# Performance work log

Hardware: AMD Instinct MI355X
Metric: run time of the kernel (lower is better)

Reference implementation:

```python
import math
import jax, jax.numpy as jnp
import numpy as np

B, T, S, H, L, NH = 2, 512, 2048, 768, 32, 12
INTERMED = 4 * H


def _make_pe(max_len, hidden):
    position = np.arange(max_len)[:, None].astype(np.float32)
    div_term = np.exp(np.arange(0, hidden, 2).astype(np.float32) * (-math.log(10000.0) / hidden))
    pe = np.zeros((max_len, hidden), dtype=np.float32)
    pe[:, 0::2] = np.sin(position * div_term)
    pe[:, 1::2] = np.cos(position * div_term)
    return jnp.asarray(pe)


def setup_inputs() -> dict:
    key = jax.random.key(0)
    ks = jax.random.split(key, 10)
    token_reps = jax.random.normal(ks[0], (B, T, H), dtype=jnp.float32)
    starts = jax.random.randint(ks[1], (B, S), 0, T - L)
    lens = jax.random.randint(ks[2], (B, S), 1, L + 1)
    span_ids = jnp.stack([starts, starts + lens], axis=-1)  # (B,S,2)
    span_masks = jax.random.uniform(ks[3], (B, S)) > 0.2
    pe = _make_pe(T, H)
    dummy_query = jax.random.normal(ks[4], (H,), dtype=jnp.float32) * 0.02
    in_proj_w = jax.random.normal(ks[5], (3 * H, H), dtype=jnp.float32) * 0.02
    in_proj_b = jnp.zeros((3 * H,), jnp.float32)
    out_proj_w = jax.random.normal(ks[6], (H, H), dtype=jnp.float32) * 0.02
    out_proj_b = jnp.zeros((H,), jnp.float32)
    norm_g = jnp.ones((H,), jnp.float32)
    norm_b = jnp.zeros((H,), jnp.float32)
    ffn_w1 = jax.random.normal(ks[7], (INTERMED, H), dtype=jnp.float32) * (math.sqrt(2.0 / H))
    ffn_b1 = jnp.zeros((INTERMED,), jnp.float32)
    ffn_w2 = jax.random.normal(ks[8], (H, INTERMED), dtype=jnp.float32) * (math.sqrt(2.0 / INTERMED))
    ffn_b2 = jnp.zeros((H,), jnp.float32)
    return dict(token_reps=token_reps, span_ids=span_ids, span_masks=span_masks,
                pooling=0, pe=pe, dummy_query=dummy_query,
                in_proj_w=in_proj_w, in_proj_b=in_proj_b,
                out_proj_w=out_proj_w, out_proj_b=out_proj_b,
                norm_g=norm_g, norm_b=norm_b,
                ffn_w1=ffn_w1, ffn_b1=ffn_b1, ffn_w2=ffn_w2, ffn_b2=ffn_b2)


def _layernorm(x, g, b, eps=1e-5):
    mu = jnp.mean(x, axis=-1, keepdims=True)
    var = jnp.mean(jnp.square(x - mu), axis=-1, keepdims=True)
    return (x - mu) * jax.lax.rsqrt(var + eps) * g + b


def reference(token_reps, span_ids, span_masks, pooling, pe, dummy_query,
              in_proj_w, in_proj_b, out_proj_w, out_proj_b,
              norm_g, norm_b, ffn_w1, ffn_b1, ffn_w2, ffn_b2):
    b, t, h = token_reps.shape
    s = span_ids.shape[1]
    hd = h // NH
    # positional encoding over the sequence (dropout=0 / eval mode)
    x = token_reps + pe[:t]
    # ragged -> padded gather of span tokens
    starts = span_ids[..., 0]
    lens = (span_ids[..., 1] - starts) * span_masks.astype(span_ids.dtype)  # (B,S)
    ar = jnp.arange(L)
    pos = starts[..., None] + ar                     # (B,S,L)
    valid = ar[None, None, :] < lens[..., None]      # (B,S,L) True = real token
    idx = jnp.clip(pos, 0, t - 1)
    gathered = jax.vmap(lambda xb, ib: xb[ib])(x, idx)   # (B,S,L,H)
    gathered = gathered * valid[..., None]
    # guard fully-masked rows (masked-out / zero-len spans): keep one key valid,
    # output is zeroed at the end anyway (matches torch span_reps[~mask]=0)
    any_v = jnp.any(valid, axis=-1)
    valid = valid.at[..., 0].set(valid[..., 0] | ~any_v)
    # single-query multi-head attention (torch nn.MultiheadAttention math)
    Wq, Wk, Wv = jnp.split(in_proj_w, 3, axis=0)
    bq, bk, bv = jnp.split(in_proj_b, 3, axis=0)
    q = (dummy_query @ Wq.T + bq).reshape(NH, hd)                  # (NH,hd)
    k = (gathered @ Wk.T + bk).reshape(b, s, L, NH, hd)
    v = (gathered @ Wv.T + bv).reshape(b, s, L, NH, hd)
    scores = jnp.einsum('nd,bslnd->bsnl', q, k) / math.sqrt(hd)    # (B,S,NH,L)
    scores = jnp.where(valid[:, :, None, :], scores, -jnp.inf)
    attn = jax.nn.softmax(scores, axis=-1)
    ctx = jnp.einsum('bsnl,bslnd->bsnd', attn, v).reshape(b, s, h)
    attn_out = ctx @ out_proj_w.T + out_proj_b
    # residual + LayerNorm, FFN, residual + same LayerNorm
    x1 = _layernorm(attn_out + dummy_query, norm_g, norm_b)
    ffn = jax.nn.relu(x1 @ ffn_w1.T + ffn_b1) @ ffn_w2.T + ffn_b2
    out = _layernorm(ffn + x1, norm_g, norm_b)
    out = out * span_masks[..., None]
    return out
```

## Files before the change

### kernel.cpp

```cpp
#include <hip/hip_runtime.h>
#include <math.h>

static constexpr int B_  = 2;
static constexpr int T_  = 512;
static constexpr int S_  = 2048;
static constexpr int H_  = 768;
static constexpr int L_  = 32;
static constexpr int NH_ = 12;
static constexpr int HD_ = 64;
static constexpr int IM_ = 3072;

typedef __bf16 bf16x8 __attribute__((ext_vector_type(8)));
typedef float  f32x4  __attribute__((ext_vector_type(4)));

__device__ __forceinline__ float bf2f(unsigned short u) {
    return __uint_as_float(((unsigned)u) << 16);
}
__device__ __forceinline__ unsigned short f2bf(float f) {
    unsigned u = __float_as_uint(f);
    u += 0x7fffu + ((u >> 16) & 1u);
    return (unsigned short)(u >> 16);
}
__device__ __forceinline__ void gl_lds16(const void* g, void* l) {
    __builtin_amdgcn_global_load_lds((const __attribute__((address_space(1))) void*)g,
                                     (__attribute__((address_space(3))) void*)l, 16, 0, 0);
}

__global__ void k_q(const float* __restrict__ dq, const float* __restrict__ w,
                    const float* __restrict__ b, float* __restrict__ q,
                    const int* __restrict__ raw, int* __restrict__ mout) {
    int wv = threadIdx.x >> 6, lane = threadIdx.x & 63;
    int i = blockIdx.x * 4 + wv;
    const float* row = w + (size_t)i * H_;
    float acc = 0.f;
#pragma unroll
    for (int k = 0; k < 12; ++k) acc += dq[lane + 64 * k] * row[lane + 64 * k];
    for (int m = 32; m; m >>= 1) acc += __shfl_xor(acc, m, 64);
    if (lane == 0) q[i] = acc + b[i];
    if (blockIdx.x == 0) {
        __shared__ int bad;
        if (threadIdx.x == 0) bad = 0;
        __syncthreads();
        for (int t = threadIdx.x; t < 1024; t += 256) {
            int v = raw[t];
            if (v != 0 && v != 1) bad = 1;
        }
        __syncthreads();
        int byte_layout = bad;
        const unsigned char* rb = (const unsigned char*)raw;
        for (int t = threadIdx.x; t < B_ * S_; t += 256)
            mout[t] = byte_layout ? (int)rb[t] : raw[t];
    }
}

static constexpr int CWB = 2880;
__global__ void k_castw(const float* __restrict__ s0, const float* __restrict__ s1,
                        const float* __restrict__ s2, const float* __restrict__ s3,
                        unsigned short* __restrict__ d0, unsigned short* __restrict__ d1,
                        unsigned short* __restrict__ d2, unsigned short* __restrict__ d3,
                        const float* __restrict__ q, const float* __restrict__ wk,
                        float* __restrict__ wq) {
    if (blockIdx.x >= CWB) {
        int i = (blockIdx.x - CWB) * 256 + threadIdx.x;
        int n = i / H_, hh = i % H_;
        float acc = 0.f;
        for (int d = 0; d < HD_; ++d)
            acc += q[n * HD_ + d] * wk[(size_t)(H_ + n * HD_ + d) * H_ + hh];
        wq[i] = acc;
        return;
    }
    const long n0 = (long)H_ * H_, n2 = (long)IM_ * H_;
    long gid = (long)(blockIdx.x * 256 + threadIdx.x) * 8;
    const float* s; unsigned short* d; long off;
    if (gid < n0)                { s = s0; d = d0; off = gid; }
    else if (gid < 2 * n0)       { s = s1; d = d1; off = gid - n0; }
    else if (gid < 2 * n0 + n2)  { s = s2; d = d2; off = gid - 2 * n0; }
    else                         { s = s3; d = d3; off = gid - 2 * n0 - n2; }
    float4 f0 = *(const float4*)(s + off);
    float4 f1 = *(const float4*)(s + off + 4);
    uint4 o;
    o.x = (unsigned)f2bf(f0.x) | ((unsigned)f2bf(f0.y) << 16);
    o.y = (unsigned)f2bf(f0.z) | ((unsigned)f2bf(f0.w) << 16);
    o.z = (unsigned)f2bf(f1.x) | ((unsigned)f2bf(f1.y) << 16);
    o.w = (unsigned)f2bf(f1.z) | ((unsigned)f2bf(f1.w) << 16);
    *(uint4*)(d + off) = o;
}

__global__ void k_xstok(const float* __restrict__ tr, const float* __restrict__ pe,
                        const float* __restrict__ wq,
                        unsigned short* __restrict__ xbf, float* __restrict__ stok) {
    __shared__ float sx[H_];
    int bt = blockIdx.x, tid = threadIdx.x;
    const float* trow = tr + (size_t)bt * H_;
    const float* prow = pe + (size_t)(bt % T_) * H_;
    if (tid < 192) {
        int h0 = tid * 4;
        float4 a = *(const float4*)(trow + h0);
        float4 p = *(const float4*)(prow + h0);
        float v0 = a.x + p.x, v1 = a.y + p.y, v2 = a.z + p.z, v3 = a.w + p.w;
        sx[h0] = v0; sx[h0 + 1] = v1; sx[h0 + 2] = v2; sx[h0 + 3] = v3;
        uint2 o;
        o.x = (unsigned)f2bf(v0) | ((unsigned)f2bf(v1) << 16);
        o.y = (unsigned)f2bf(v2) | ((unsigned)f2bf(v3) << 16);
        *(uint2*)(xbf + (size_t)bt * H_ + h0) = o;
    }
    __syncthreads();
    int lane = tid & 63, w = tid >> 6;
    float xv[12];
#pragma unroll
    for (int k = 0; k < 12; ++k) xv[k] = sx[lane + 64 * k];
#pragma unroll
    for (int hh = 0; hh < 3; ++hh) {
        int n = w * 3 + hh;
        const float* wr = wq + (size_t)n * H_;
        float acc = 0.f;
#pragma unroll
        for (int k = 0; k < 12; ++k) acc += xv[k] * wr[lane + 64 * k];
        for (int m = 32; m; m >>= 1) acc += __shfl_xor(acc, m, 64);
        if (lane == 0) stok[bt * NH_ + n] = acc;
    }
}

__global__ void k_castv4(const unsigned short* __restrict__ p, size_t pstr,
                         unsigned short* __restrict__ dst, int n) {
    int i = (blockIdx.x * 256 + threadIdx.x) * 8;
    if (i >= n) return;
    float a[8] = {};
#pragma unroll
    for (int z = 0; z < 4; ++z) {
        uint4 u = *(const uint4*)(p + z * pstr + i);
        a[0] += bf2f((unsigned short)(u.x & 0xffff));
        a[1] += bf2f((unsigned short)(u.x >> 16));
        a[2] += bf2f((unsigned short)(u.y & 0xffff));
        a[3] += bf2f((unsigned short)(u.y >> 16));
        a[4] += bf2f((unsigned short)(u.z & 0xffff));
        a[5] += bf2f((unsigned short)(u.z >> 16));
        a[6] += bf2f((unsigned short)(u.w & 0xffff));
        a[7] += bf2f((unsigned short)(u.w >> 16));
    }
    uint4 o;
    o.x = (unsigned)f2bf(a[0]) | ((unsigned)f2bf(a[1]) << 16);
    o.y = (unsigned)f2bf(a[2]) | ((unsigned)f2bf(a[3]) << 16);
    o.z = (unsigned)f2bf(a[4]) | ((unsigned)f2bf(a[5]) << 16);
    o.w = (unsigned)f2bf(a[6]) | ((unsigned)f2bf(a[7]) << 16);
    *(uint4*)(dst + i) = o;
}

template <bool RELU, bool SPLIT>
__global__ __launch_bounds__(256)
void gemm_bt(const unsigned short* __restrict__ A, const unsigned short* __restrict__ W,
             const float* __restrict__ bias, unsigned short* __restrict__ Cout,
             int M, int N, int K, int kLen, int TX, int SP) {
    __shared__ unsigned short As[4096];
    __shared__ unsigned short Bs[4096];
    const int qx = blockIdx.x & 7, t = blockIdx.x >> 3;
    const int gi = t / TX, x = t - gi * TX;
    const int g = gi * 8 + qx;
    int y, z;
    if (SPLIT) { y = g / SP; z = g - y * SP; } else { y = g; z = 0; }
    const int bm = y * 128, bn = x * 128;
    const int kOff = z * kLen;

    const int tid = threadIdx.x, lane = tid & 63, wid = tid >> 6;
    const int wm = (wid >> 1) * 64, wn = (wid & 1) * 64;
    const int r16 = lane >> 2, c4 = lane & 3;
    const int swc = (c4 ^ ((r16 >> 1) & 3)) * 8;
    const unsigned short* agp = A + (size_t)(bm + wid * 32 + r16) * K + kOff + swc;
    const unsigned short* bgp = W + (size_t)(bn + wid * 32 + r16) * K + kOff + swc;
    unsigned short* lA = As + wid * 1024;
    unsigned short* lB = Bs + wid * 1024;

    f32x4 acc[4][4];
#pragma unroll
    for (int i = 0; i < 4; ++i)
#pragma unroll
        for (int j = 0; j < 4; ++j) acc[i][j] = f32x4{0.f, 0.f, 0.f, 0.f};

    const int mrow = lane & 15;
    const int q4 = lane >> 4;
    const int sw = (q4 ^ ((mrow >> 1) & 3)) * 8;
    const int NIT = kLen >> 5;

    for (int it = 0; it < NIT; ++it) {
        const int k0 = it << 5;
        gl_lds16(agp + k0, lA);
        gl_lds16(agp + (size_t)16 * K + k0, lA + 512);
        gl_lds16(bgp + k0, lB);
        gl_lds16(bgp + (size_t)16 * K + k0, lB + 512);
        __syncthreads();
        bf16x8 af[4], bfr[4];
#pragma unroll
        for (int i = 0; i < 4; ++i)
            af[i] = *(const bf16x8*)(As + (wm + i * 16 + mrow) * 32 + sw);
#pragma unroll
        for (int j = 0; j < 4; ++j)
            bfr[j] = *(const bf16x8*)(Bs + (wn + j * 16 + mrow) * 32 + sw);
#pragma unroll
        for (int i = 0; i < 4; ++i)
#pragma unroll
            for (int j = 0; j < 4; ++j)
                acc[i][j] = __builtin_amdgcn_mfma_f32_16x16x32_bf16(af[i], bfr[j], acc[i][j], 0, 0, 0);
        __syncthreads();
    }

    const bool addb = !SPLIT || z == 0;
    unsigned short* outp = SPLIT ? Cout + (size_t)z * M * N : Cout;
    const int lr = (lane >> 4) * 4, lc = lane & 15;
#pragma unroll
    for (int j = 0; j < 4; ++j) {
        int col = bn + wn + j * 16 + lc;
        float bv = addb ? bias[col] : 0.f;
#pragma unroll
        for (int i = 0; i < 4; ++i) {
            int row0 = bm + wm + i * 16 + lr;
#pragma unroll
            for (int r = 0; r < 4; ++r) {
                float v = acc[i][j][r] + bv;
                if (RELU) v = fmaxf(v, 0.f);
                outp[(size_t)(row0 + r) * N + col] = f2bf(v);
            }
        }
    }
}

__global__ void k_attn(const float* __restrict__ stok, const unsigned short* __restrict__ vtok,
                       const int* __restrict__ span_ids, const int* __restrict__ masks,
                       unsigned short* __restrict__ ctx) {
    int r = blockIdx.x, b = r / S_;
    unsigned short* out = ctx + (size_t)r * H_;
    int tid = threadIdx.x;
    __shared__ float w[NH_][L_];
    __shared__ int idxs[L_];
    __shared__ int s_len;
    if (tid == 0) {
        int m = masks[r];
        int st = span_ids[2 * r], en = span_ids[2 * r + 1];
        int len = m ? (en - st) : 0;
        len = len < 0 ? 0 : (len > L_ ? L_ : len);
        s_len = len;
    }
    __syncthreads();
    int len = s_len;
    if (len == 0) {
        for (int h2 = tid; h2 < H_ / 2; h2 += 256) ((unsigned*)out)[h2] = 0u;
        return;
    }
    if (tid < L_) {
        int p = span_ids[2 * r] + tid;
        idxs[tid] = p < 0 ? 0 : (p > T_ - 1 ? T_ - 1 : p);
    }
    __syncthreads();
    for (int i = tid; i < NH_ * L_; i += 256) {
        int n = i / L_, l = i % L_;
        w[n][l] = (l < len) ? stok[(size_t)(b * T_ + idxs[l]) * NH_ + n] * 0.125f : -INFINITY;
    }
    __syncthreads();
    if (tid < NH_) {
        float mx = -INFINITY;
        for (int l = 0; l < len; ++l) mx = fmaxf(mx, w[tid][l]);
        float sum = 0.f;
        for (int l = 0; l < len; ++l) { float e = __expf(w[tid][l] - mx); w[tid][l] = e; sum += e; }
        float inv = 1.f / sum;
        for (int l = 0; l < len; ++l) w[tid][l] *= inv;
    }
    __syncthreads();
    if (tid < 192) {
        int h0 = tid * 4, n = h0 >> 6;
        float a0 = 0.f, a1 = 0.f, a2 = 0.f, a3 = 0.f;
        for (int l = 0; l < len; ++l) {
            float wl = w[n][l];
            const unsigned short* vr = vtok + (size_t)(b * T_ + idxs[l]) * H_ + h0;
            uint2 u = *(const uint2*)vr;
            a0 += wl * bf2f((unsigned short)(u.x & 0xffff));
            a1 += wl * bf2f((unsigned short)(u.x >> 16));
            a2 += wl * bf2f((unsigned short)(u.y & 0xffff));
            a3 += wl * bf2f((unsigned short)(u.y >> 16));
        }
        uint2 o;
        o.x = (unsigned)f2bf(a0) | ((unsigned)f2bf(a1) << 16);
        o.y = (unsigned)f2bf(a2) | ((unsigned)f2bf(a3) << 16);
        *(uint2*)(out + h0) = o;
    }
}

template <bool RESROW, bool MASKOUT>
__global__ void k_ln(const unsigned short* __restrict__ parts, size_t pstr,
                     const float* __restrict__ resf, const unsigned short* __restrict__ resb,
                     const float* __restrict__ g, const float* __restrict__ bt,
                     float* __restrict__ outf, unsigned short* __restrict__ outb,
                     const int* __restrict__ masks) {
    int r = blockIdx.x;
    int tid = threadIdx.x;
    float v[3];
    float lsum = 0.f;
#pragma unroll
    for (int i = 0; i < 3; ++i) {
        int h = tid + 256 * i;
        float s = RESROW ? bf2f(resb[(size_t)r * H_ + h]) : resf[h];
#pragma unroll
        for (int z = 0; z < 4; ++z)
            s += bf2f(parts[z * pstr + (size_t)r * H_ + h]);
        v[i] = s;
        lsum += s;
    }
    __shared__ float sh[256];
    sh[tid] = lsum;
    __syncthreads();
    for (int st = 128; st > 0; st >>= 1) {
        if (tid < st) sh[tid] += sh[tid + st];
        __syncthreads();
    }
    float mean = sh[0] * (1.f / H_);
    __syncthreads();
    float lvar = 0.f;
#pragma unroll
    for (int i = 0; i < 3; ++i) { float d = v[i] - mean; lvar += d * d; }
    sh[tid] = lvar;
    __syncthreads();
    for (int st = 128; st > 0; st >>= 1) {
        if (tid < st) sh[tid] += sh[tid + st];
        __syncthreads();
    }
    float var = sh[0] * (1.f / H_);
    float scale = rsqrtf(var + 1e-5f);
    float mfac = 1.f;
    if (MASKOUT) mfac = masks[r] ? 1.f : 0.f;
#pragma unroll
    for (int i = 0; i < 3; ++i) {
        int h = tid + 256 * i;
        float o = ((v[i] - mean) * scale * g[h] + bt[h]) * mfac;
        if (MASKOUT) outf[(size_t)r * H_ + h] = o;
        else         outb[(size_t)r * H_ + h] = f2bf(o);
    }
}

extern "C" void kernel_launch(void* const* d_in, const int* in_sizes, int n_in,
                              void* d_out, int out_size, void* d_ws, size_t ws_size,
                              hipStream_t stream) {
    const float* token_reps = (const float*)d_in[0];
    const int*   span_ids   = (const int*)d_in[1];
    const int*   masks_raw  = (const int*)d_in[2];
    const float* pe   = (const float*)d_in[4];
    const float* dq   = (const float*)d_in[5];
    const float* in_w = (const float*)d_in[6];
    const float* in_b = (const float*)d_in[7];
    const float* ow   = (const float*)d_in[8];
    const float* ob   = (const float*)d_in[9];
    const float* g    = (const float*)d_in[10];
    const float* bt   = (const float*)d_in[11];
    const float* w1   = (const float*)d_in[12];
    const float* b1   = (const float*)d_in[13];
    const float* w2   = (const float*)d_in[14];
    const float* b2   = (const float*)d_in[15];

    const int BS = B_ * S_;
    const int BT = B_ * T_;

    float* fws   = (float*)d_ws;
    float* stok  = fws;
    float* qv    = stok + BT * NH_;
    float* wqeff = qv + H_;
    unsigned short* us = (unsigned short*)(wqeff + NH_ * H_);
    unsigned short* pbuf = us;
    unsigned short* xbf  = pbuf + (size_t)4 * BS * H_;
    unsigned short* vtok = xbf + (size_t)BT * H_;
    unsigned short* ctx  = vtok + (size_t)BT * H_;
    unsigned short* x1bf = ctx + (size_t)BS * H_;
    unsigned short* f1   = x1bf + (size_t)BS * H_;
    unsigned short* wvb  = f1 + (size_t)BS * IM_;
    unsigned short* owb  = wvb + H_ * H_;
    unsigned short* w1b  = owb + H_ * H_;
    unsigned short* w2b  = w1b + IM_ * H_;
    int* maskn = (int*)(w2b + H_ * IM_);

    k_q<<<H_ / 4, 256, 0, stream>>>(dq, in_w, in_b, qv, masks_raw, maskn);
    k_castw<<<CWB + 36, 256, 0, stream>>>(
        in_w + (size_t)2 * H_ * H_, ow, w1, w2, wvb, owb, w1b, w2b,
        qv, in_w, wqeff);
    k_xstok<<<BT, 256, 0, stream>>>(token_reps, pe, wqeff, xbf, stok);
    gemm_bt<false, true><<<192, 256, 0, stream>>>(
        xbf, wvb, in_b + 2 * H_, pbuf, BT, H_, H_, H_ / 4, 6, 4);
    k_castv4<<<(BT * H_ / 8 + 255) / 256, 256, 0, stream>>>(
        pbuf, (size_t)BT * H_, vtok, BT * H_);
    k_attn<<<BS, 256, 0, stream>>>(stok, vtok, span_ids, maskn, ctx);
    gemm_bt<false, true><<<768, 256, 0, stream>>>(
        ctx, owb, ob, pbuf, BS, H_, H_, H_ / 4, 6, 4);
    k_ln<false, false><<<BS, 256, 0, stream>>>(
        pbuf, (size_t)BS * H_, dq, nullptr, g, bt, nullptr, x1bf, nullptr);
    gemm_bt<true, false><<<768, 256, 0, stream>>>(
        x1bf, w1b, b1, f1, BS, IM_, H_, H_, 24, 1);
    gemm_bt<false, true><<<768, 256, 0, stream>>>(
        f1, w2b, b2, pbuf, BS, H_, IM_, IM_ / 4, 6, 4);
    k_ln<true, true><<<BS, 256, 0, stream>>>(
        pbuf, (size_t)BS * H_, nullptr, x1bf, g, bt, (float*)d_out, nullptr, maskn);
}
```

Before: 241.4 us.

## Add 256x256-tile ping-pong pipelined GEMM for the FFN layers

```diff
diff --git a/kernel.cpp b/kernel.cpp
--- a/kernel.cpp
+++ b/kernel.cpp
@@ -212,6 +212,163 @@
         float bv = addb ? bias[col] : 0.f;
 #pragma unroll
         for (int i = 0; i < 4; ++i) {
+            int row0 = bm + wm + i * 16 + lr;
+#pragma unroll
+            for (int r = 0; r < 4; ++r) {
+                float v = acc[i][j][r] + bv;
+                if (RELU) v = fmaxf(v, 0.f);
+                outp[(size_t)(row0 + r) * N + col] = f2bf(v);
+            }
+        }
+    }
+}
+
+#define STG(gp_, lp_, h_, kt_) do {                                           \
+    const unsigned short* _g = (gp_) + (size_t)((h_) * 128) * K + (kt_) * 64; \
+    unsigned short* _l = (lp_) + (h_) * (128 * 64);                           \
+    gl_lds16(_g, _l);                                                         \
+    gl_lds16(_g + (size_t)8 * K, _l + 8 * 64);                                \
+} while (0)
+
+#define LDF(dst_, mat_, rowoff_, kk_)                                         \
+    dst_ = *(const bf16x8*)((const char*)(mat_) + (rowoff_) * 128 + rbase +   \
+                            ((kk_) ? c1 : c0))
+
+#define RD_A(mat_, base_) do {                                                \
+    LDF(a_[0][0], mat_, (base_) + 0,  0); LDF(a_[0][1], mat_, (base_) + 0,  1); \
+    LDF(a_[1][0], mat_, (base_) + 16, 0); LDF(a_[1][1], mat_, (base_) + 16, 1); \
+    LDF(a_[2][0], mat_, (base_) + 32, 0); LDF(a_[2][1], mat_, (base_) + 32, 1); \
+    LDF(a_[3][0], mat_, (base_) + 48, 0); LDF(a_[3][1], mat_, (base_) + 48, 1); \
+} while (0)
+
+#define RD_B(dst_, mat_, base_) do {                                          \
+    LDF(dst_[0][0], mat_, (base_) + 0,  0); LDF(dst_[0][1], mat_, (base_) + 0,  1); \
+    LDF(dst_[1][0], mat_, (base_) + 16, 0); LDF(dst_[1][1], mat_, (base_) + 16, 1); \
+} while (0)
+
+#define QPH(MH_, NH_, B_) do {                                                \
+    _Pragma("unroll")                                                         \
+    for (int m_ = 0; m_ < 4; ++m_) {                                          \
+        _Pragma("unroll")                                                     \
+        for (int n_ = 0; n_ < 2; ++n_) {                                      \
+            f32x4 c_ = acc[(MH_) * 4 + m_][(NH_) * 2 + n_];                   \
+            c_ = __builtin_amdgcn_mfma_f32_16x16x32_bf16(a_[m_][0], B_[n_][0], c_, 0, 0, 0); \
+            c_ = __builtin_amdgcn_mfma_f32_16x16x32_bf16(a_[m_][1], B_[n_][1], c_, 0, 0, 0); \
+            acc[(MH_) * 4 + m_][(NH_) * 2 + n_] = c_;                         \
+        }                                                                     \
+    }                                                                         \
+} while (0)
+
+#define PH_MID do {                                                           \
+    __builtin_amdgcn_s_barrier();                                             \
+    asm volatile("s_waitcnt lgkmcnt(0)" ::: "memory");                        \
+    __builtin_amdgcn_sched_barrier(0);                                        \
+    __builtin_amdgcn_s_setprio(1);                                            \
+} while (0)
+
+#define PH_END do {                                                           \
+    __builtin_amdgcn_s_setprio(0);                                            \
+    __builtin_amdgcn_s_barrier();                                             \
+    __builtin_amdgcn_sched_barrier(0);                                        \
+} while (0)
+
+#define PH_ENDV do {                                                          \
+    __builtin_amdgcn_s_setprio(0);                                            \
+    asm volatile("s_waitcnt vmcnt(4)" ::: "memory");                          \
+    __builtin_amdgcn_s_barrier();                                             \
+    __builtin_amdgcn_sched_barrier(0);                                        \
+} while (0)
+
+template <bool RELU, bool SPLIT>
+__global__ __launch_bounds__(512)
+void gemm256(const unsigned short* __restrict__ A, const unsigned short* __restrict__ W,
+             const float* __restrict__ bias, unsigned short* __restrict__ Cout,
+             int M, int N, int K, int kLen, int NTt, int SP) {
+    __shared__ unsigned short lds[4][256 * 64];
+    (void)SP;
+    const int MT = M >> 8;
+    int bid = blockIdx.x;
+    int z = 0, rem = bid;
+    if (SPLIT) { int tpz = MT * NTt; z = bid / tpz; rem = bid - z * tpz; }
+    const int y = rem / NTt, x = rem - y * NTt;
+    const int bm = y * 256, bn = x * 256;
+    const int kOff = z * kLen;
+    const int NT = kLen >> 6;
+    const int NIT2 = NT >> 1;
+
+    const int tid = threadIdx.x, lane = tid & 63, wid = tid >> 6;
+    const int wm = (wid >> 2) * 128, wn = (wid & 3) * 64;
+    const int mrow = lane & 15, q4 = lane >> 4;
+    const int rbase = mrow * 128;
+    const int c0 = (q4 ^ (mrow & 7)) * 16;
+    const int c1 = ((4 + q4) ^ (mrow & 7)) * 16;
+
+    const int srow = wid * 16 + (lane >> 3);
+    const int gcol = ((lane & 7) ^ ((lane >> 3) & 7)) * 8;
+    const unsigned short* agp = A + (size_t)(bm + srow) * K + kOff + gcol;
+    const unsigned short* bgp = W + (size_t)(bn + srow) * K + kOff + gcol;
+    unsigned short* const aLp0 = lds[0] + wid * 1024;
+    unsigned short* const bLp0 = lds[1] + wid * 1024;
+    unsigned short* const aLp1 = lds[2] + wid * 1024;
+    unsigned short* const bLp1 = lds[3] + wid * 1024;
+
+    f32x4 acc[8][4];
+#pragma unroll
+    for (int i = 0; i < 8; ++i)
+#pragma unroll
+        for (int j = 0; j < 4; ++j) acc[i][j] = f32x4{0.f, 0.f, 0.f, 0.f};
+
+    bf16x8 a_[4][2], b0_[2][2], b1_[2][2];
+
+    STG(agp, aLp0, 0, 0);
+    STG(agp, aLp0, 1, 0);
+    STG(bgp, bLp0, 0, 0);
+    STG(bgp, bLp0, 1, 0);
+    STG(bgp, bLp1, 0, 1);
+    STG(agp, aLp1, 0, 1);
+    asm volatile("s_waitcnt vmcnt(4)" ::: "memory");
+    __builtin_amdgcn_s_barrier();
+    __builtin_amdgcn_sched_barrier(0);
+
+    for (int t = 0; t < NIT2; ++t) {
+        const int k1 = 2 * t + 1;
+        int k2 = 2 * t + 2; if (k2 > NT - 1) k2 = NT - 1;
+        int k3 = 2 * t + 3; if (k3 > NT - 1) k3 = NT - 1;
+        RD_A(lds[0], wm);
+        RD_B(b0_, lds[1], wn);
+        STG(bgp, bLp1, 1, k1);
+        PH_MID; QPH(0, 0, b0_); PH_END;
+        RD_B(b1_, lds[1], wn + 32);
+        STG(agp, aLp1, 1, k1);
+        PH_MID; QPH(0, 1, b1_); PH_END;
+        RD_A(lds[0], wm + 64);
+        STG(bgp, bLp0, 0, k2);
+        PH_MID; QPH(1, 0, b0_); PH_END;
+        STG(agp, aLp0, 0, k2);
+        PH_MID; QPH(1, 1, b1_); PH_ENDV;
+        RD_A(lds[2], wm);
+        RD_B(b0_, lds[3], wn);
+        STG(bgp, bLp0, 1, k2);
+        PH_MID; QPH(0, 0, b0_); PH_END;
+        RD_B(b1_, lds[3], wn + 32);
+        STG(agp, aLp0, 1, k2);
+        PH_MID; QPH(0, 1, b1_); PH_END;
+        RD_A(lds[2], wm + 64);
+        STG(bgp, bLp1, 0, k3);
+        PH_MID; QPH(1, 0, b0_); PH_END;
+        STG(agp, aLp1, 0, k3);
+        PH_MID; QPH(1, 1, b1_); PH_ENDV;
+    }
+
+    const bool addb = !SPLIT || z == 0;
+    unsigned short* outp = SPLIT ? Cout + (size_t)z * M * N : Cout;
+    const int lr = (lane >> 4) * 4, lc = lane & 15;
+#pragma unroll
+    for (int j = 0; j < 4; ++j) {
+        int col = bn + wn + j * 16 + lc;
+        float bv = addb ? bias[col] : 0.f;
+#pragma unroll
+        for (int i = 0; i < 8; ++i) {
             int row0 = bm + wm + i * 16 + lr;
 #pragma unroll
             for (int r = 0; r < 4; ++r) {
@@ -387,10 +544,10 @@
         ctx, owb, ob, pbuf, BS, H_, H_, H_ / 4, 6, 4);
     k_ln<false, false><<<BS, 256, 0, stream>>>(
         pbuf, (size_t)BS * H_, dq, nullptr, g, bt, nullptr, x1bf, nullptr);
-    gemm_bt<true, false><<<768, 256, 0, stream>>>(
-        x1bf, w1b, b1, f1, BS, IM_, H_, H_, 24, 1);
-    gemm_bt<false, true><<<768, 256, 0, stream>>>(
-        f1, w2b, b2, pbuf, BS, H_, IM_, IM_ / 4, 6, 4);
+    gemm256<true, false><<<192, 512, 0, stream>>>(
+        x1bf, w1b, b1, f1, BS, IM_, H_, H_, IM_ / 256, 1);
+    gemm256<false, true><<<192, 512, 0, stream>>>(
+        f1, w2b, b2, pbuf, BS, H_, IM_, IM_ / 4, H_ / 256, 4);
     k_ln<true, true><<<BS, 256, 0, stream>>>(
         pbuf, (size_t)BS * H_, nullptr, x1bf, g, bt, (float*)d_out, nullptr, maskn);
 }
```

Result: no change. 244.3 us (+1.2%).

## Double-buffer GEMM LDS tiles and halve split-K for oproj and FFN2

Applied to the files above, without the earlier changes.

```diff
diff --git a/kernel.cpp b/kernel.cpp
--- a/kernel.cpp
+++ b/kernel.cpp
@@ -146,13 +146,20 @@
     *(uint4*)(dst + i) = o;
 }
 
+#define STG2(c_, k0e_) do {                                                   \
+    gl_lds16(agp + (k0e_), lA + (c_) * 4096);                                 \
+    gl_lds16(agp + (size_t)16 * K + (k0e_), lA + (c_) * 4096 + 512);          \
+    gl_lds16(bgp + (k0e_), lB + (c_) * 4096);                                 \
+    gl_lds16(bgp + (size_t)16 * K + (k0e_), lB + (c_) * 4096 + 512);          \
+} while (0)
+
 template <bool RELU, bool SPLIT>
-__global__ __launch_bounds__(256)
-void gemm_bt(const unsigned short* __restrict__ A, const unsigned short* __restrict__ W,
-             const float* __restrict__ bias, unsigned short* __restrict__ Cout,
-             int M, int N, int K, int kLen, int TX, int SP) {
-    __shared__ unsigned short As[4096];
-    __shared__ unsigned short Bs[4096];
+__device__ __forceinline__
+void gemm_db_body(const unsigned short* __restrict__ A, const unsigned short* __restrict__ W,
+                  const float* __restrict__ bias, unsigned short* __restrict__ Cout,
+                  int M, int N, int K, int kLen, int TX, int SP) {
+    __shared__ unsigned short As[2][4096];
+    __shared__ unsigned short Bs[2][4096];
     const int qx = blockIdx.x & 7, t = blockIdx.x >> 3;
     const int gi = t / TX, x = t - gi * TX;
     const int g = gi * 8 + qx;
@@ -167,8 +174,8 @@
     const int swc = (c4 ^ ((r16 >> 1) & 3)) * 8;
     const unsigned short* agp = A + (size_t)(bm + wid * 32 + r16) * K + kOff + swc;
     const unsigned short* bgp = W + (size_t)(bn + wid * 32 + r16) * K + kOff + swc;
-    unsigned short* lA = As + wid * 1024;
-    unsigned short* lB = Bs + wid * 1024;
+    unsigned short* lA = &As[0][0] + wid * 1024;
+    unsigned short* lB = &Bs[0][0] + wid * 1024;
 
     f32x4 acc[4][4];
 #pragma unroll
@@ -181,27 +188,34 @@
     const int sw = (q4 ^ ((mrow >> 1) & 3)) * 8;
     const int NIT = kLen >> 5;
 
+    STG2(0, 0);
     for (int it = 0; it < NIT; ++it) {
-        const int k0 = it << 5;
-        gl_lds16(agp + k0, lA);
-        gl_lds16(agp + (size_t)16 * K + k0, lA + 512);
-        gl_lds16(bgp + k0, lB);
-        gl_lds16(bgp + (size_t)16 * K + k0, lB + 512);
-        __syncthreads();
+        const int cur = it & 1;
+        int nk = it + 1; if (nk >= NIT) nk = NIT - 1;
+        STG2(cur ^ 1, nk << 5);
+        asm volatile("s_waitcnt vmcnt(4)" ::: "memory");
+        __builtin_amdgcn_s_barrier();
+        __builtin_amdgcn_sched_barrier(0);
+        const unsigned short* Ac = &As[cur][0];
+        const unsigned short* Bc = &Bs[cur][0];
         bf16x8 af[4], bfr[4];
 #pragma unroll
         for (int i = 0; i < 4; ++i)
-            af[i] = *(const bf16x8*)(As + (wm + i * 16 + mrow) * 32 + sw);
+            af[i] = *(const bf16x8*)(Ac + (wm + i * 16 + mrow) * 32 + sw);
 #pragma unroll
         for (int j = 0; j < 4; ++j)
-            bfr[j] = *(const bf16x8*)(Bs + (wn + j * 16 + mrow) * 32 + sw);
+            bfr[j] = *(const bf16x8*)(Bc + (wn + j * 16 + mrow) * 32 + sw);
+        asm volatile("s_waitcnt lgkmcnt(0)" ::: "memory");
+        __builtin_amdgcn_sched_barrier(0);
 #pragma unroll
         for (int i = 0; i < 4; ++i)
 #pragma unroll
             for (int j = 0; j < 4; ++j)
                 acc[i][j] = __builtin_amdgcn_mfma_f32_16x16x32_bf16(af[i], bfr[j], acc[i][j], 0, 0, 0);
-        __syncthreads();
-    }
+        __builtin_amdgcn_s_barrier();
+        __builtin_amdgcn_sched_barrier(0);
+    }
+    asm volatile("s_waitcnt vmcnt(0)" ::: "memory");
 
     const bool addb = !SPLIT || z == 0;
     unsigned short* outp = SPLIT ? Cout + (size_t)z * M * N : Cout;
@@ -221,6 +235,27 @@
             }
         }
     }
+}
+
+__global__ __launch_bounds__(256)
+void g2_vtok(const unsigned short* A, const unsigned short* W, const float* bias,
+             unsigned short* Cout, int M, int N, int K, int kLen, int TX, int SP) {
+    gemm_db_body<false, true>(A, W, bias, Cout, M, N, K, kLen, TX, SP);
+}
+__global__ __launch_bounds__(256)
+void g2_oproj(const unsigned short* A, const unsigned short* W, const float* bias,
+              unsigned short* Cout, int M, int N, int K, int kLen, int TX, int SP) {
+    gemm_db_body<false, true>(A, W, bias, Cout, M, N, K, kLen, TX, SP);
+}
+__global__ __launch_bounds__(256)
+void g2_ffn1(const unsigned short* A, const unsigned short* W, const float* bias,
+             unsigned short* Cout, int M, int N, int K, int kLen, int TX, int SP) {
+    gemm_db_body<true, false>(A, W, bias, Cout, M, N, K, kLen, TX, SP);
+}
+__global__ __launch_bounds__(256)
+void g2_ffn2(const unsigned short* A, const unsigned short* W, const float* bias,
+             unsigned short* Cout, int M, int N, int K, int kLen, int TX, int SP) {
+    gemm_db_body<false, true>(A, W, bias, Cout, M, N, K, kLen, TX, SP);
 }
 
 __global__ void k_attn(const float* __restrict__ stok, const unsigned short* __restrict__ vtok,
@@ -283,7 +318,7 @@
     }
 }
 
-template <bool RESROW, bool MASKOUT>
+template <bool RESROW, bool MASKOUT, int ZN>
 __global__ void k_ln(const unsigned short* __restrict__ parts, size_t pstr,
                      const float* __restrict__ resf, const unsigned short* __restrict__ resb,
                      const float* __restrict__ g, const float* __restrict__ bt,
@@ -298,7 +333,7 @@
         int h = tid + 256 * i;
         float s = RESROW ? bf2f(resb[(size_t)r * H_ + h]) : resf[h];
 #pragma unroll
-        for (int z = 0; z < 4; ++z)
+        for (int z = 0; z < ZN; ++z)
             s += bf2f(parts[z * pstr + (size_t)r * H_ + h]);
         v[i] = s;
         lsum += s;
@@ -378,19 +413,19 @@
         in_w + (size_t)2 * H_ * H_, ow, w1, w2, wvb, owb, w1b, w2b,
         qv, in_w, wqeff);
     k_xstok<<<BT, 256, 0, stream>>>(token_reps, pe, wqeff, xbf, stok);
-    gemm_bt<false, true><<<192, 256, 0, stream>>>(
+    g2_vtok<<<192, 256, 0, stream>>>(
         xbf, wvb, in_b + 2 * H_, pbuf, BT, H_, H_, H_ / 4, 6, 4);
     k_castv4<<<(BT * H_ / 8 + 255) / 256, 256, 0, stream>>>(
         pbuf, (size_t)BT * H_, vtok, BT * H_);
     k_attn<<<BS, 256, 0, stream>>>(stok, vtok, span_ids, maskn, ctx);
-    gemm_bt<false, true><<<768, 256, 0, stream>>>(
-        ctx, owb, ob, pbuf, BS, H_, H_, H_ / 4, 6, 4);
-    k_ln<false, false><<<BS, 256, 0, stream>>>(
+    g2_oproj<<<384, 256, 0, stream>>>(
+        ctx, owb, ob, pbuf, BS, H_, H_, H_ / 2, 6, 2);
+    k_ln<false, false, 2><<<BS, 256, 0, stream>>>(
         pbuf, (size_t)BS * H_, dq, nullptr, g, bt, nullptr, x1bf, nullptr);
-    gemm_bt<true, false><<<768, 256, 0, stream>>>(
+    g2_ffn1<<<768, 256, 0, stream>>>(
         x1bf, w1b, b1, f1, BS, IM_, H_, H_, 24, 1);
-    gemm_bt<false, true><<<768, 256, 0, stream>>>(
-        f1, w2b, b2, pbuf, BS, H_, IM_, IM_ / 4, 6, 4);
-    k_ln<true, true><<<BS, 256, 0, stream>>>(
+    g2_ffn2<<<384, 256, 0, stream>>>(
+        f1, w2b, b2, pbuf, BS, H_, IM_, IM_ / 2, 6, 2);
+    k_ln<true, true, 2><<<BS, 256, 0, stream>>>(
         pbuf, (size_t)BS * H_, nullptr, x1bf, g, bt, (float*)d_out, nullptr, maskn);
 }
```

Measured after the change: 243.5 us. Within noise of the previous version (+0.9%).
